# Performance work log

Measured on AMD Instinct MI355X. Metric: run time of the kernel, lower is better.

Reference implementation:

```python
import jax, jax.numpy as jnp
import numpy as np
import math

B, S, E, H = 2, 4096, 1024, 16
W = 256  # one-sided attention window (attention_window // 2)


def setup_inputs() -> dict:
    key = jax.random.key(0)
    ks = jax.random.split(key, 7)
    init = lambda k, shp: jax.random.normal(k, shp, jnp.float32) * 0.02
    return {
        "hidden_states": jax.random.normal(ks[0], (B, S, E), jnp.float32),
        "attention_mask": jnp.zeros((B, S), jnp.int32),  # 0 = local attention
        "q_w": init(ks[1], (E, E)), "q_b": jnp.zeros((E,), jnp.float32),
        "k_w": init(ks[2], (E, E)), "k_b": jnp.zeros((E,), jnp.float32),
        "v_w": init(ks[3], (E, E)), "v_b": jnp.zeros((E,), jnp.float32),
    }


def _banded_attention(hidden_states, attention_mask, q_w, q_b, k_w, k_b, v_w, v_b):
    D = E // H          # head dim
    w = W               # one-sided window
    nc = S // w         # number of query chunks of length w
    # Projections (torch Linear: x @ W.T + b); query pre-scaled by sqrt(head_dim)
    q = (hidden_states @ q_w.T + q_b) / math.sqrt(D)
    k = hidden_states @ k_w.T + k_b
    v = hidden_states @ v_w.T + v_b
    heads = lambda x: x.reshape(B, S, H, D).transpose(0, 2, 1, 3)  # [B,H,S,D]
    q, k, v = heads(q), heads(k), heads(v)

    qc = q.reshape(B, H, nc, w, D)                       # [B,H,nc,w,D]
    pad = lambda x: jnp.pad(x, ((0, 0), (0, 0), (w, w), (0, 0)))
    # chunk c of keys/values covers padded positions [c*w, c*w + 3w)
    idx = (jnp.arange(nc) * w)[:, None] + jnp.arange(3 * w)[None, :]  # [nc,3w]
    kc = pad(k)[:, :, idx]                               # [B,H,nc,3w,D]
    vc = pad(v)[:, :, idx]                               # [B,H,nc,3w,D]

    # banded scores: query x in chunk attends padded key y; rel offset = y-w-x
    scores = jnp.einsum('bhcxd,bhcyd->bhcxy', qc, kc)    # [B,H,nc,w,3w]

    # additive mask from attention_mask (!=0 -> -10000 at that key position)
    fm = jnp.where(attention_mask != 0, -10000.0, 0.0)   # [B,S]
    fmc = jnp.pad(fm, ((0, 0), (w, w)))[:, idx]          # [B,nc,3w]
    scores = scores + fmc[:, None, :, None, :]

    # validity: |rel| <= w (the 2w+1 band) and key index j in [0, S)
    x = jnp.arange(w)[:, None]                           # [w,1]
    y = jnp.arange(3 * w)[None, :]                       # [1,3w]
    rel = y - w - x                                      # [w,3w]
    j = (jnp.arange(nc) * w)[:, None, None] + (y - w)[None]  # [nc,1,3w] key idx
    valid = (jnp.abs(rel) <= w)[None] & (j >= 0) & (j < S)   # [nc,w,3w]
    scores = jnp.where(valid[None, None], scores, -jnp.inf)

    probs = jax.nn.softmax(scores.astype(jnp.float32), axis=-1)
    ctx = jnp.einsum('bhcxy,bhcyd->bhcxd', probs, vc)    # [B,H,nc,w,D]
    return ctx.reshape(B, H, S, D).transpose(0, 2, 1, 3).reshape(B, S, E)


def reference(hidden_states, attention_mask, q_w, q_b, k_w, k_b, v_w, v_b):
    return _banded_attention(hidden_states, attention_mask,
                             q_w, q_b, k_w, k_b, v_w, v_b)
```

## Files before the change

kernel.cpp:

```cpp
#include <hip/hip_runtime.h>
#include <math.h>

constexpr int Bn  = 2;
constexpr int Sn  = 4096;
constexpr int En  = 1024;
constexpr int Hn  = 16;
constexpr int Mtot = Bn * Sn;
constexpr int Kp  = 1024;
constexpr int PAD = 72;

typedef __bf16    bf16x8 __attribute__((ext_vector_type(8)));
typedef __bf16    bf16x4 __attribute__((ext_vector_type(4)));
typedef _Float16  f16x8  __attribute__((ext_vector_type(8)));
typedef _Float16  f16x4  __attribute__((ext_vector_type(4)));
typedef float     f32x4  __attribute__((ext_vector_type(4)));

__global__ void __launch_bounds__(256)
cvt_hs_kernel(const float* __restrict__ hs, _Float16* __restrict__ hs16)
{
    int t = blockIdx.x * 256 + threadIdx.x;
    int m = t >> 8;
    int k = (t & 255) << 2;
    float4 x = *(const float4*)&hs[((size_t)m << 10) + k];
    f16x4 h;
    h[0] = (_Float16)x.x; h[1] = (_Float16)x.y;
    h[2] = (_Float16)x.z; h[3] = (_Float16)x.w;
    *(f16x4*)&hs16[((size_t)m << 10) + k] = h;
}

__global__ void __launch_bounds__(256)
cvt_w_kernel(const float* __restrict__ qw, const float* __restrict__ kw,
             const float* __restrict__ vw, _Float16* __restrict__ w16)
{
    int t = blockIdx.x * 256 + threadIdx.x;
    int gn = t >> 8;
    int k  = (t & 255) << 2;
    int p  = gn >> 10, n = gn & 1023;
    const float* src = (p == 0) ? qw : (p == 1) ? kw : vw;
    float4 x = *(const float4*)&src[((size_t)n << 10) + k];
    f16x4 h;
    h[0] = (_Float16)x.x; h[1] = (_Float16)x.y;
    h[2] = (_Float16)x.z; h[3] = (_Float16)x.w;
    *(f16x4*)&w16[((size_t)gn << 10) + k] = h;
}

__device__ inline void load_lds16(const void* g, void* s) {
    __builtin_amdgcn_global_load_lds((const __attribute__((address_space(1))) void*)g,
                                     (__attribute__((address_space(3))) void*)s,
                                     16, 0, 0);
}

template<int PM>
__global__ void __launch_bounds__(256)
qkv_mfma_kernel(const _Float16* __restrict__ A2, const _Float16* __restrict__ B2,
                const float* __restrict__ qb, const float* __restrict__ kb,
                const float* __restrict__ vb,
                __bf16* __restrict__ q16, __bf16* __restrict__ k16,
                __bf16* __restrict__ vt16, int n0base)
{
    __shared__ _Float16 As[128 * 32];
    __shared__ _Float16 Bs[128 * 32];

    const int tid  = threadIdx.x;
    const int m0   = blockIdx.x * 128;
    const int n0   = n0base + blockIdx.y * 128;
    const int w    = tid >> 6;
    const int lane = tid & 63;
    const int wm   = w >> 1, wn = w & 1;
    const int mrow = lane & 15, quad = lane >> 4;

    const int stRow = w * 16 + (lane >> 2);
    const int stCol = ((lane & 3) ^ ((lane >> 3) & 3)) * 8;
    const int rq = (quad ^ ((mrow >> 1) & 3)) * 8;

    f32x4 acc[4][4] = {};

    const _Float16* Abase = A2 + (size_t)(m0 + stRow) * Kp + stCol;
    const _Float16* Bbase = B2 + (size_t)(n0 + stRow) * Kp + stCol;
    _Float16* AsW = &As[w * 512];
    _Float16* BsW = &Bs[w * 512];

    for (int k0 = 0; k0 < Kp; k0 += 32) {
        load_lds16(Abase + k0,            AsW);
        load_lds16(Abase + 64 * Kp + k0,  AsW + 2048);
        load_lds16(Bbase + k0,            BsW);
        load_lds16(Bbase + 64 * Kp + k0,  BsW + 2048);
        __syncthreads();
        f16x8 af[4], bfr[4];
#pragma unroll
        for (int t = 0; t < 4; t++) {
            af[t]  = *(const f16x8*)&As[(wm * 64 + t * 16 + mrow) * 32 + rq];
            bfr[t] = *(const f16x8*)&Bs[(wn * 64 + t * 16 + mrow) * 32 + rq];
        }
#pragma unroll
        for (int ti = 0; ti < 4; ti++)
#pragma unroll
            for (int tj = 0; tj < 4; tj++) {
                if (PM == 0)
                    acc[ti][tj] = __builtin_amdgcn_mfma_f32_16x16x32_f16(
                        bfr[tj], af[ti], acc[ti][tj], 0, 0, 0);
                else
                    acc[ti][tj] = __builtin_amdgcn_mfma_f32_16x16x32_f16(
                        af[ti], bfr[tj], acc[ti][tj], 0, 0, 0);
            }
        __syncthreads();
    }

    if (PM == 0) {
        const int p = n0 >> 10;
        const float* bptr = (p == 0) ? qb : kb;
        __bf16* dst = (p == 0) ? q16 : k16;
        const float scl = (p == 0) ? 0.125f : 1.0f;
#pragma unroll
        for (int ti = 0; ti < 4; ti++) {
            const int m  = m0 + wm * 64 + ti * 16 + mrow;
            const int bb = m >> 12, ss = m & 4095;
#pragma unroll
            for (int tj = 0; tj < 4; tj++) {
                const int fl = (n0 + wn * 64 + tj * 16 + quad * 4) & 1023;
                const int hh = fl >> 6, dd = fl & 63;
                const float4 bv = *(const float4*)&bptr[fl];
                bf16x4 o;
                o[0] = (__bf16)((acc[ti][tj][0] + bv.x) * scl);
                o[1] = (__bf16)((acc[ti][tj][1] + bv.y) * scl);
                o[2] = (__bf16)((acc[ti][tj][2] + bv.z) * scl);
                o[3] = (__bf16)((acc[ti][tj][3] + bv.w) * scl);
                *(bf16x4*)&dst[((size_t)(bb * Hn + hh) * Sn + ss) * 64 + dd] = o;
            }
        }
    } else {
#pragma unroll
        for (int tj = 0; tj < 4; tj++) {
            const int n  = n0 + wn * 64 + tj * 16 + mrow;
            const float bv = vb[n & 1023];
            const int hh = (n & 1023) >> 6, dd = n & 63;
#pragma unroll
            for (int ti = 0; ti < 4; ti++) {
                const int m  = m0 + wm * 64 + ti * 16 + quad * 4;
                const int bb = m >> 12, ss = m & 4095;
                bf16x4 pv4;
#pragma unroll
                for (int r = 0; r < 4; r++)
                    pv4[r] = (__bf16)(acc[ti][tj][r] + bv);
                *(bf16x4*)&vt16[((size_t)(bb * Hn + hh) * 64 + dd) * Sn + ss] = pv4;
            }
        }
    }
}

__global__ void __launch_bounds__(256, 2)
banded_attn_kernel(const __bf16* __restrict__ q16, const __bf16* __restrict__ k16,
                   const __bf16* __restrict__ vt16, const int* __restrict__ mask,
                   float* __restrict__ out)
{
    __shared__ __bf16 Kt[2][64 * PAD];
    __shared__ __bf16 Vt[2][64 * PAD];
    __shared__ __bf16 Pt[4][64 * PAD];
    __shared__ float  Msh[768];

    const int c = blockIdx.x, h = blockIdx.y, b = blockIdx.z;
    const int bh = b * Hn + h;
    const int i0 = c * 256;
    const int jwin0 = i0 - 256;
    const int tid  = threadIdx.x;
    const int wv   = tid >> 6;
    const int lane = tid & 63;
    const int quad = lane >> 4, mrow = lane & 15;

#pragma unroll
    for (int rep = 0; rep < 3; rep++) {
        int idx = rep * 256 + tid;
        int jg  = jwin0 + idx;
        float mv = 0.f;
        if (jg >= 0 && jg < Sn && mask[b * Sn + jg] != 0) mv = -10000.f;
        Msh[idx] = mv;
    }

    bf16x8 qf[4][2];
    const __bf16* qbase = q16 + (((size_t)bh * Sn + i0 + wv * 64) << 6);
#pragma unroll
    for (int tjq = 0; tjq < 4; tjq++)
#pragma unroll
        for (int kc = 0; kc < 2; kc++)
            qf[tjq][kc] = *(const bf16x8*)(qbase + (16 * tjq + mrow) * 64 + 32 * kc + 8 * quad);

    const int sr = lane >> 3;
    const int sc = lane & 7;
    bf16x8 kreg0, kreg1, vreg0, vreg1;
    auto gload = [&](int st) {
        const int j0 = jwin0 + st * 64;
        const int r0 = wv * 16 + sr;
        const int r1 = wv * 16 + 8 + sr;
        int jk0 = j0 + r0; jk0 = jk0 < 0 ? 0 : (jk0 > Sn - 1 ? Sn - 1 : jk0);
        int jk1 = j0 + r1; jk1 = jk1 < 0 ? 0 : (jk1 > Sn - 1 ? Sn - 1 : jk1);
        kreg0 = *(const bf16x8*)&k16[(((size_t)bh * Sn + jk0) << 6) + sc * 8];
        kreg1 = *(const bf16x8*)&k16[(((size_t)bh * Sn + jk1) << 6) + sc * 8];
        int jv = j0 + sc * 8; jv = jv < 0 ? 0 : (jv > Sn - 8 ? Sn - 8 : jv);
        vreg0 = *(const bf16x8*)&vt16[((size_t)bh * 64 + r0) * Sn + jv];
        vreg1 = *(const bf16x8*)&vt16[((size_t)bh * 64 + r1) * Sn + jv];
    };
    auto swrite = [&](int buf) {
        *(bf16x8*)&Kt[buf][(wv * 16 + sr) * PAD + sc * 8]     = kreg0;
        *(bf16x8*)&Kt[buf][(wv * 16 + 8 + sr) * PAD + sc * 8] = kreg1;
        *(bf16x8*)&Vt[buf][(wv * 16 + sr) * PAD + sc * 8]     = vreg0;
        *(bf16x8*)&Vt[buf][(wv * 16 + 8 + sr) * PAD + sc * 8] = vreg1;
    };

    f32x4 acc_o[4][4] = {};
    float lrun[4] = {0.f, 0.f, 0.f, 0.f};
    __bf16* Pw = &Pt[wv][0];

    gload(0);
    swrite(0);
    __syncthreads();

    for (int st = 0; st < 12; st++) {
        const int buf = st & 1;
        if (st + 1 < 12) gload(st + 1);

        if (st >= wv && st <= wv + 8) {
            const __bf16* KtB = &Kt[buf][0];
            const __bf16* VtB = &Vt[buf][0];
#pragma unroll
            for (int ti = 0; ti < 4; ti++) {
                bf16x8 ak0 = *(const bf16x8*)&KtB[(16 * ti + mrow) * PAD + quad * 8];
                bf16x8 ak1 = *(const bf16x8*)&KtB[(16 * ti + mrow) * PAD + 32 + quad * 8];
                const int y0 = 64 * st + 16 * ti + 4 * quad;
                f32x4 ms4 = *(const f32x4*)&Msh[y0];
#pragma unroll
                for (int tjq = 0; tjq < 4; tjq++) {
                    f32x4 s = {};
                    s = __builtin_amdgcn_mfma_f32_16x16x32_bf16(ak0, qf[tjq][0], s, 0, 0, 0);
                    s = __builtin_amdgcn_mfma_f32_16x16x32_bf16(ak1, qf[tjq][1], s, 0, 0, 0);
                    const int xq = 64 * wv + 16 * tjq + mrow;
                    bf16x4 pk;
                    float psum = 0.f;
#pragma unroll
                    for (int r = 0; r < 4; r++) {
                        const int y = y0 + r;
                        bool ok = ((unsigned)(y - xq) <= 512u) &
                                  ((unsigned)(jwin0 + y) < 4096u);
                        float pv = ok ? __expf(s[r] + ms4[r]) : 0.f;
                        psum += pv;
                        pk[r] = (__bf16)pv;
                    }
                    lrun[tjq] += psum;
                    *(bf16x4*)&Pw[(16 * tjq + mrow) * PAD + 16 * ti + 4 * quad] = pk;
                }
            }
#pragma unroll
            for (int kc2 = 0; kc2 < 2; kc2++) {
                bf16x8 av[4];
#pragma unroll
                for (int dt = 0; dt < 4; dt++)
                    av[dt] = *(const bf16x8*)&VtB[(16 * dt + mrow) * PAD + kc2 * 32 + quad * 8];
#pragma unroll
                for (int tjq = 0; tjq < 4; tjq++) {
                    bf16x8 pf = *(const bf16x8*)&Pw[(16 * tjq + mrow) * PAD + kc2 * 32 + quad * 8];
#pragma unroll
                    for (int dt = 0; dt < 4; dt++)
                        acc_o[dt][tjq] = __builtin_amdgcn_mfma_f32_16x16x32_bf16(
                            av[dt], pf, acc_o[dt][tjq], 0, 0, 0);
                }
            }
        }

        if (st + 1 < 12) {
            swrite((st + 1) & 1);
            __syncthreads();
        }
    }

    float inv[4];
#pragma unroll
    for (int tjq = 0; tjq < 4; tjq++) {
        float l = lrun[tjq];
        l += __shfl_xor(l, 16);
        l += __shfl_xor(l, 32);
        inv[tjq] = 1.0f / l;
    }
#pragma unroll
    for (int dt = 0; dt < 4; dt++)
#pragma unroll
        for (int tjq = 0; tjq < 4; tjq++) {
            f32x4 o = acc_o[dt][tjq];
            o[0] *= inv[tjq]; o[1] *= inv[tjq]; o[2] *= inv[tjq]; o[3] *= inv[tjq];
            float* dst = out + ((size_t)(b * Sn + i0 + wv * 64 + 16 * tjq + mrow)) * En
                             + h * 64 + 16 * dt + 4 * quad;
            *(f32x4*)dst = o;
        }
}

extern "C" void kernel_launch(void* const* d_in, const int* in_sizes, int n_in,
                              void* d_out, int out_size, void* d_ws, size_t ws_size,
                              hipStream_t stream) {
    const float* hs  = (const float*)d_in[0];
    const int*  mask = (const int*)d_in[1];
    const float* qw  = (const float*)d_in[2];
    const float* qb  = (const float*)d_in[3];
    const float* kw  = (const float*)d_in[4];
    const float* kb  = (const float*)d_in[5];
    const float* vw  = (const float*)d_in[6];
    const float* vb  = (const float*)d_in[7];
    float* out = (float*)d_out;

    _Float16* hs16 = (_Float16*)d_ws;
    _Float16* w16  = (_Float16*)((char*)d_ws + (size_t)16777216);
    __bf16*   q16  = (__bf16*)((char*)d_ws + (size_t)23068672);
    __bf16*   k16  = (__bf16*)((char*)d_ws + (size_t)39845888);
    __bf16*   vt16 = (__bf16*)((char*)d_ws + (size_t)56623104);

    cvt_hs_kernel<<<8192, 256, 0, stream>>>(hs, hs16);
    cvt_w_kernel <<<3072, 256, 0, stream>>>(qw, kw, vw, w16);

    dim3 pgridQK(Mtot / 128, 2048 / 128);
    qkv_mfma_kernel<0><<<pgridQK, 256, 0, stream>>>(hs16, w16, qb, kb, vb,
                                                    q16, k16, vt16, 0);
    dim3 pgridV(Mtot / 128, 1024 / 128);
    qkv_mfma_kernel<1><<<pgridV, 256, 0, stream>>>(hs16, w16, qb, kb, vb,
                                                   q16, k16, vt16, 2048);

    dim3 agrid(Sn / 256, Hn, Bn);
    banded_attn_kernel<<<agrid, 256, 0, stream>>>(q16, k16, vt16, mask, out);
}
```

Measured before the change: 221.1 us.

## Triple-buffer LDS in QKV GEMM with async prefetch and manual waitcnt

Replaces the single-buffered load/sync/compute loop in the QKV projection GEMM with a three-stage LDS ring. Tiles two steps ahead are issued with global_load_lds while the current tile is consumed, using explicit vmcnt waits and raw barriers instead of full __syncthreads. It also raises wave priority around the MFMA block. The goal is to hide global-memory latency behind matrix math, at the cost of tripling LDS use (which may lower occupancy) and relying on hand-written waitcnt correctness.

Measured after the change: 227.2 us. +2.8%, slower.

```diff
diff --git a/kernel.cpp b/kernel.cpp
--- a/kernel.cpp
+++ b/kernel.cpp
@@ -58,8 +58,8 @@
                 __bf16* __restrict__ q16, __bf16* __restrict__ k16,
                 __bf16* __restrict__ vt16, int n0base)
 {
-    __shared__ _Float16 As[128 * 32];
-    __shared__ _Float16 Bs[128 * 32];
+    __shared__ _Float16 As[3][128 * 32];
+    __shared__ _Float16 Bs[3][128 * 32];
 
     const int tid  = threadIdx.x;
     const int m0   = blockIdx.x * 128;
@@ -77,21 +77,27 @@
 
     const _Float16* Abase = A2 + (size_t)(m0 + stRow) * Kp + stCol;
     const _Float16* Bbase = B2 + (size_t)(n0 + stRow) * Kp + stCol;
-    _Float16* AsW = &As[w * 512];
-    _Float16* BsW = &Bs[w * 512];
-
-    for (int k0 = 0; k0 < Kp; k0 += 32) {
+
+    auto stage = [&](int t, int bi) {
+        const int k0 = t * 32;
+        _Float16* AsW = &As[bi][w * 512];
+        _Float16* BsW = &Bs[bi][w * 512];
         load_lds16(Abase + k0,            AsW);
         load_lds16(Abase + 64 * Kp + k0,  AsW + 2048);
         load_lds16(Bbase + k0,            BsW);
         load_lds16(Bbase + 64 * Kp + k0,  BsW + 2048);
-        __syncthreads();
+    };
+
+    auto compute = [&](int bi) {
         f16x8 af[4], bfr[4];
+        const _Float16* AsR = &As[bi][0];
+        const _Float16* BsR = &Bs[bi][0];
 #pragma unroll
         for (int t = 0; t < 4; t++) {
-            af[t]  = *(const f16x8*)&As[(wm * 64 + t * 16 + mrow) * 32 + rq];
-            bfr[t] = *(const f16x8*)&Bs[(wn * 64 + t * 16 + mrow) * 32 + rq];
-        }
+            af[t]  = *(const f16x8*)&AsR[(wm * 64 + t * 16 + mrow) * 32 + rq];
+            bfr[t] = *(const f16x8*)&BsR[(wn * 64 + t * 16 + mrow) * 32 + rq];
+        }
+        __builtin_amdgcn_s_setprio(1);
 #pragma unroll
         for (int ti = 0; ti < 4; ti++)
 #pragma unroll
@@ -103,8 +109,32 @@
                     acc[ti][tj] = __builtin_amdgcn_mfma_f32_16x16x32_f16(
                         af[ti], bfr[tj], acc[ti][tj], 0, 0, 0);
             }
-        __syncthreads();
-    }
+        __builtin_amdgcn_s_setprio(0);
+    };
+
+    stage(0, 0);
+    stage(1, 1);
+    int bcur = 0;
+    int bpre = 2;
+    for (int t = 0; t < 30; ++t) {
+        stage(t + 2, bpre);
+        asm volatile("s_waitcnt vmcnt(8)" ::: "memory");
+        __builtin_amdgcn_s_barrier();
+        compute(bcur);
+        asm volatile("s_waitcnt lgkmcnt(0)" ::: "memory");
+        __builtin_amdgcn_s_barrier();
+        bpre = bcur;
+        bcur = (bcur == 2) ? 0 : bcur + 1;
+    }
+    asm volatile("s_waitcnt vmcnt(4)" ::: "memory");
+    __builtin_amdgcn_s_barrier();
+    compute(bcur);
+    asm volatile("s_waitcnt lgkmcnt(0)" ::: "memory");
+    __builtin_amdgcn_s_barrier();
+    bcur = (bcur == 2) ? 0 : bcur + 1;
+    asm volatile("s_waitcnt vmcnt(0)" ::: "memory");
+    __builtin_amdgcn_s_barrier();
+    compute(bcur);
 
     if (PM == 0) {
         const int p = n0 >> 10;
```

## Rework QKV GEMM to 256x256 tiles with double-buffered LDS pipeline

Applied to the files above, without the earlier changes.

The QKV projection GEMM moves from 128x128 tiles with 256 threads and K-step 32 to 256x256 tiles with 512 threads, K-step 64 and double-buffered LDS. The next tile's global-to-LDS loads are issued between MFMA ladders, using raw barriers and setprio to overlap memory traffic with matrix math. A new XOR swizzle is used for 64-wide rows. The goal is more data reuse per load and hidden load latency, at the cost of 128KB of LDS per block, heavy register pressure from 32 accumulators, and fewer blocks for the V GEMM (128 blocks).

Result: slower. 229.7 us (+3.9%).

```diff
diff --git a/kernel.cpp b/kernel.cpp
--- a/kernel.cpp
+++ b/kernel.cpp
@@ -50,60 +50,122 @@
                                      16, 0, 0);
 }
 
+__device__ inline void block_sync() {
+    asm volatile("" ::: "memory");
+    __builtin_amdgcn_s_barrier();
+    asm volatile("" ::: "memory");
+}
+__device__ inline void block_sync_vm0() {
+    asm volatile("s_waitcnt vmcnt(0)" ::: "memory");
+    __builtin_amdgcn_s_barrier();
+    asm volatile("" ::: "memory");
+}
+
 template<int PM>
-__global__ void __launch_bounds__(256)
+__global__ void __launch_bounds__(512, 2)
 qkv_mfma_kernel(const _Float16* __restrict__ A2, const _Float16* __restrict__ B2,
                 const float* __restrict__ qb, const float* __restrict__ kb,
                 const float* __restrict__ vb,
                 __bf16* __restrict__ q16, __bf16* __restrict__ k16,
                 __bf16* __restrict__ vt16, int n0base)
 {
-    __shared__ _Float16 As[128 * 32];
-    __shared__ _Float16 Bs[128 * 32];
+    __shared__ _Float16 As[2][256 * 64];
+    __shared__ _Float16 Bs[2][256 * 64];
 
     const int tid  = threadIdx.x;
-    const int m0   = blockIdx.x * 128;
-    const int n0   = n0base + blockIdx.y * 128;
     const int w    = tid >> 6;
     const int lane = tid & 63;
-    const int wm   = w >> 1, wn = w & 1;
+    const int wm   = w >> 2, wn = w & 3;
     const int mrow = lane & 15, quad = lane >> 4;
-
-    const int stRow = w * 16 + (lane >> 2);
-    const int stCol = ((lane & 3) ^ ((lane >> 3) & 3)) * 8;
-    const int rq = (quad ^ ((mrow >> 1) & 3)) * 8;
-
-    f32x4 acc[4][4] = {};
-
-    const _Float16* Abase = A2 + (size_t)(m0 + stRow) * Kp + stCol;
-    const _Float16* Bbase = B2 + (size_t)(n0 + stRow) * Kp + stCol;
-    _Float16* AsW = &As[w * 512];
-    _Float16* BsW = &Bs[w * 512];
-
-    for (int k0 = 0; k0 < Kp; k0 += 32) {
-        load_lds16(Abase + k0,            AsW);
-        load_lds16(Abase + 64 * Kp + k0,  AsW + 2048);
-        load_lds16(Bbase + k0,            BsW);
-        load_lds16(Bbase + 64 * Kp + k0,  BsW + 2048);
-        __syncthreads();
-        f16x8 af[4], bfr[4];
-#pragma unroll
-        for (int t = 0; t < 4; t++) {
-            af[t]  = *(const f16x8*)&As[(wm * 64 + t * 16 + mrow) * 32 + rq];
-            bfr[t] = *(const f16x8*)&Bs[(wn * 64 + t * 16 + mrow) * 32 + rq];
-        }
+    const int m0   = blockIdx.x * 256;
+    const int n0   = n0base + blockIdx.y * 256;
+
+    const int subrow = lane >> 3;
+    const int g8     = ((lane & 7) ^ subrow) * 8;
+    const _Float16* Ag = A2 + (size_t)(m0 + w * 32 + subrow) * Kp + g8;
+    const _Float16* Bg = B2 + (size_t)(n0 + w * 32 + subrow) * Kp + g8;
+
+    const int arow = wm * 128 + mrow;
+    const int brow = wn * 64 + mrow;
+    const int cx   = quad ^ (mrow & 7);
+
+    f32x4 acc[8][4] = {};
+
+    auto stageA = [&](int kt, int bi) {
+        const int k0 = kt * 64;
+#pragma unroll
+        for (int l = 0; l < 4; l++)
+            load_lds16(Ag + (size_t)l * 8 * Kp + k0, &As[bi][(w * 32 + l * 8) * 64]);
+    };
+    auto stageB = [&](int kt, int bi) {
+        const int k0 = kt * 64;
+#pragma unroll
+        for (int l = 0; l < 4; l++)
+            load_lds16(Bg + (size_t)l * 8 * Kp + k0, &Bs[bi][(w * 32 + l * 8) * 64]);
+    };
+    auto ladder = [&](const f16x8* AF, const f16x8* BF, int r0) {
+        __builtin_amdgcn_s_setprio(1);
 #pragma unroll
         for (int ti = 0; ti < 4; ti++)
 #pragma unroll
             for (int tj = 0; tj < 4; tj++) {
                 if (PM == 0)
-                    acc[ti][tj] = __builtin_amdgcn_mfma_f32_16x16x32_f16(
-                        bfr[tj], af[ti], acc[ti][tj], 0, 0, 0);
+                    acc[r0 + ti][tj] = __builtin_amdgcn_mfma_f32_16x16x32_f16(
+                        BF[tj], AF[ti], acc[r0 + ti][tj], 0, 0, 0);
                 else
-                    acc[ti][tj] = __builtin_amdgcn_mfma_f32_16x16x32_f16(
-                        af[ti], bfr[tj], acc[ti][tj], 0, 0, 0);
-            }
-        __syncthreads();
+                    acc[r0 + ti][tj] = __builtin_amdgcn_mfma_f32_16x16x32_f16(
+                        AF[ti], BF[tj], acc[r0 + ti][tj], 0, 0, 0);
+            }
+        __builtin_amdgcn_s_setprio(0);
+    };
+
+    constexpr int NT = Kp / 64;
+
+    stageA(0, 0);
+    stageB(0, 0);
+    block_sync_vm0();
+
+    for (int kt = 0; kt < NT; ++kt) {
+        const int rb = kt & 1, wb = rb ^ 1;
+        const _Float16* AsR = &As[rb][0];
+        const _Float16* BsR = &Bs[rb][0];
+        f16x8 af[4], bf[4];
+
+#pragma unroll
+        for (int t = 0; t < 4; t++)
+            af[t] = *(const f16x8*)&AsR[(arow + t * 16) * 64 + cx * 8];
+#pragma unroll
+        for (int t = 0; t < 4; t++)
+            bf[t] = *(const f16x8*)&BsR[(brow + t * 16) * 64 + cx * 8];
+        if (kt + 1 < NT) stageA(kt + 1, wb);
+        block_sync();
+        ladder(af, bf, 0);
+        block_sync();
+
+#pragma unroll
+        for (int t = 0; t < 4; t++)
+            af[t] = *(const f16x8*)&AsR[(arow + 64 + t * 16) * 64 + cx * 8];
+        if (kt + 1 < NT) stageB(kt + 1, wb);
+        block_sync();
+        ladder(af, bf, 4);
+        block_sync();
+
+#pragma unroll
+        for (int t = 0; t < 4; t++)
+            af[t] = *(const f16x8*)&AsR[(arow + t * 16) * 64 + (cx ^ 4) * 8];
+#pragma unroll
+        for (int t = 0; t < 4; t++)
+            bf[t] = *(const f16x8*)&BsR[(brow + t * 16) * 64 + (cx ^ 4) * 8];
+        block_sync();
+        ladder(af, bf, 0);
+        block_sync();
+
+#pragma unroll
+        for (int t = 0; t < 4; t++)
+            af[t] = *(const f16x8*)&AsR[(arow + 64 + t * 16) * 64 + (cx ^ 4) * 8];
+        block_sync();
+        ladder(af, bf, 4);
+        block_sync_vm0();
     }
 
     if (PM == 0) {
@@ -112,8 +174,8 @@
         __bf16* dst = (p == 0) ? q16 : k16;
         const float scl = (p == 0) ? 0.125f : 1.0f;
 #pragma unroll
-        for (int ti = 0; ti < 4; ti++) {
-            const int m  = m0 + wm * 64 + ti * 16 + mrow;
+        for (int ti = 0; ti < 8; ti++) {
+            const int m  = m0 + wm * 128 + ti * 16 + mrow;
             const int bb = m >> 12, ss = m & 4095;
 #pragma unroll
             for (int tj = 0; tj < 4; tj++) {
@@ -135,8 +197,8 @@
             const float bv = vb[n & 1023];
             const int hh = (n & 1023) >> 6, dd = n & 63;
 #pragma unroll
-            for (int ti = 0; ti < 4; ti++) {
-                const int m  = m0 + wm * 64 + ti * 16 + quad * 4;
+            for (int ti = 0; ti < 8; ti++) {
+                const int m  = m0 + wm * 128 + ti * 16 + quad * 4;
                 const int bb = m >> 12, ss = m & 4095;
                 bf16x4 pv4;
 #pragma unroll
@@ -313,11 +375,11 @@
     cvt_hs_kernel<<<8192, 256, 0, stream>>>(hs, hs16);
     cvt_w_kernel <<<3072, 256, 0, stream>>>(qw, kw, vw, w16);
 
-    dim3 pgridQK(Mtot / 128, 2048 / 128);
-    qkv_mfma_kernel<0><<<pgridQK, 256, 0, stream>>>(hs16, w16, qb, kb, vb,
+    dim3 pgridQK(Mtot / 256, 2048 / 256);
+    qkv_mfma_kernel<0><<<pgridQK, 512, 0, stream>>>(hs16, w16, qb, kb, vb,
                                                     q16, k16, vt16, 0);
-    dim3 pgridV(Mtot / 128, 1024 / 128);
-    qkv_mfma_kernel<1><<<pgridV, 256, 0, stream>>>(hs16, w16, qb, kb, vb,
+    dim3 pgridV(Mtot / 256, 1024 / 256);
+    qkv_mfma_kernel<1><<<pgridV, 512, 0, stream>>>(hs16, w16, qb, kb, vb,
                                                    q16, k16, vt16, 2048);
 
     dim3 agrid(Sn / 256, Hn, Bn);
```
